# Performance work log

Hardware: AMD Instinct MI355X
Metric: run time of the kernel (lower is better)

Reference implementation:

```python
import jax, jax.numpy as jnp
import numpy as np

NODE_DIM = 512
PROMPT_DIM = 512
N_NODES = 100000
N_GRAPHS = 1024


def setup_inputs() -> dict:
    key = jax.random.key(0)
    k1, k2, k3, k4, k5, k6, k7 = jax.random.split(key, 7)
    node_feats = jax.random.normal(k1, (N_NODES, NODE_DIM), dtype=jnp.float32)
    graph_prompt = jax.random.normal(k2, (N_GRAPHS, PROMPT_DIM), dtype=jnp.float32)
    batch_idx = jnp.sort(jax.random.randint(k3, (N_NODES,), 0, N_GRAPHS))
    # Linear init ~ U(-1/sqrt(fan_in), 1/sqrt(fan_in)) like torch defaults
    fan1 = NODE_DIM + PROMPT_DIM
    b1 = 1.0 / np.sqrt(fan1)
    W1 = jax.random.uniform(k4, (fan1, NODE_DIM), minval=-b1, maxval=b1, dtype=jnp.float32)
    bias1 = jax.random.uniform(k5, (NODE_DIM,), minval=-b1, maxval=b1, dtype=jnp.float32)
    b2 = 1.0 / np.sqrt(NODE_DIM)
    W2 = jax.random.uniform(k6, (NODE_DIM, NODE_DIM), minval=-b2, maxval=b2, dtype=jnp.float32)
    bias2 = jax.random.uniform(k7, (NODE_DIM,), minval=-b2, maxval=b2, dtype=jnp.float32)
    return {"node_feats": node_feats, "graph_prompt": graph_prompt, "batch_idx": batch_idx,
            "W1": W1, "bias1": bias1, "W2": W2, "bias2": bias2}


def reference(node_feats, graph_prompt, batch_idx, W1, bias1, W2, bias2):
    # gather per-node prompt: [N, prompt_dim]
    prompt_expanded = graph_prompt[batch_idx]
    combined = jnp.concatenate([node_feats, prompt_expanded], axis=-1)  # [N, node_dim+prompt_dim]
    h = jax.nn.relu(combined @ W1 + bias1)  # [N, node_dim]
    return h @ W2 + bias2  # [N, node_dim]
```

## Files before the change

### kernel.cpp

```cpp
#include <hip/hip_runtime.h>


#define N_NODES 100000
#define NWG 3128

typedef __bf16 bf16x8 __attribute__((ext_vector_type(8)));
typedef float  f32x4  __attribute__((ext_vector_type(4)));
typedef unsigned short ushort_t;

__device__ __forceinline__ ushort_t f2bf(float f) {
  __bf16 b = (__bf16)f;
  return __builtin_bit_cast(unsigned short, b);
}

__device__ __forceinline__ bf16x8 cvt8(const float* p) {
  float4 x = *(const float4*)p;
  float4 y = *(const float4*)(p + 4);
  bf16x8 v;
  v[0] = (__bf16)x.x; v[1] = (__bf16)x.y; v[2] = (__bf16)x.z; v[3] = (__bf16)x.w;
  v[4] = (__bf16)y.x; v[5] = (__bf16)y.y; v[6] = (__bf16)y.z; v[7] = (__bf16)y.w;
  return v;
}

__device__ __forceinline__ bf16x8 cvt8v(float4 x, float4 y) {
  bf16x8 v;
  v[0] = (__bf16)x.x; v[1] = (__bf16)x.y; v[2] = (__bf16)x.z; v[3] = (__bf16)x.w;
  v[4] = (__bf16)y.x; v[5] = (__bf16)y.y; v[6] = (__bf16)y.z; v[7] = (__bf16)y.w;
  return v;
}

__device__ __forceinline__ void gload_lds16(const void* g, void* l) {
  __builtin_amdgcn_global_load_lds(
      (const __attribute__((address_space(1))) void*)g,
      (__attribute__((address_space(3))) void*)l, 16, 0, 0);
}

__global__ void prep_kernel(const float* __restrict__ W1, const float* __restrict__ W2,
                            ushort_t* __restrict__ W1T, ushort_t* __restrict__ W2T) {
  int i = blockIdx.x * 256 + threadIdx.x;
  if (i < 524288) {
    int n = i >> 10, k = i & 1023;
    W1T[i] = f2bf(W1[k * 512 + n]);
  } else if (i < 786432) {
    int j = i - 524288;
    int n = j >> 9, k = j & 511;
    W2T[j] = f2bf(W2[k * 512 + n]);
  }
}

__global__ __launch_bounds__(256, 4) void p2_kernel(
    const float* __restrict__ gp, const ushort_t* __restrict__ W1T,
    const float* __restrict__ bias1, float* __restrict__ P2) {
  const int tid = threadIdx.x, lane = tid & 63, wid = tid >> 6;
  const int lc = lane & 15, lr = lane >> 4;
  const int m0 = (blockIdx.x >> 1) * 32;
  const int col0 = (blockIdx.x & 1) * 256 + wid * 64;

  f32x4 acc[2][4];
#pragma unroll
  for (int i = 0; i < 2; ++i)
#pragma unroll
    for (int j = 0; j < 4; ++j) acc[i][j] = {0.f, 0.f, 0.f, 0.f};

  const float* a0 = gp + (size_t)(m0 + lc) * 512;
  const ushort_t* bb = W1T + (size_t)(col0 + lc) * 1024 + 512;

#pragma unroll 2
  for (int kt = 0; kt < 8; ++kt) {
    bf16x8 bfr[2][4];
#pragma unroll
    for (int kk = 0; kk < 2; ++kk)
#pragma unroll
      for (int j = 0; j < 4; ++j)
        bfr[kk][j] = *(const bf16x8*)(bb + (size_t)j * 16 * 1024 + kt * 64 + kk * 32 + lr * 8);
    bf16x8 af[2][2];
#pragma unroll
    for (int i = 0; i < 2; ++i)
#pragma unroll
      for (int kk = 0; kk < 2; ++kk)
        af[i][kk] = cvt8(a0 + (size_t)i * 16 * 512 + kt * 64 + kk * 32 + lr * 8);
#pragma unroll
    for (int kk = 0; kk < 2; ++kk)
#pragma unroll
      for (int i = 0; i < 2; ++i)
#pragma unroll
        for (int j = 0; j < 4; ++j)
          acc[i][j] = __builtin_amdgcn_mfma_f32_16x16x32_bf16(af[i][kk], bfr[kk][j], acc[i][j], 0, 0, 0);
  }

#pragma unroll
  for (int i = 0; i < 2; ++i)
#pragma unroll
    for (int r = 0; r < 4; ++r) {
      int row = m0 + i * 16 + lr * 4 + r;
#pragma unroll
      for (int j = 0; j < 4; ++j) {
        int col = col0 + j * 16 + lc;
        P2[(size_t)row * 512 + col] = acc[i][j][r] + bias1[col];
      }
    }
}

__global__ __launch_bounds__(256, 4) void g1_kernel(
    const float* __restrict__ nf, const int* __restrict__ bidx,
    const ushort_t* __restrict__ W1T, const float* __restrict__ P2,
    ushort_t* __restrict__ h) {
  __shared__ ushort_t sA[128 * 64];
  __shared__ ushort_t sB[128 * 64];

  const int tid = threadIdx.x, lane = tid & 63, wid = tid >> 6;
  const int tile = (blockIdx.x & 7) * 391 + (blockIdx.x >> 3);
  const int m0 = (tile >> 2) * 128, n0 = (tile & 3) * 128;

  const float* pAg[4]; int ldsA[4];
#pragma unroll
  for (int s = 0; s < 4; ++s) {
    int q = s * 256 + tid;
    int row = q >> 3;
    int cw = (q & 7) ^ (row & 7);
    int rowg = m0 + row; if (rowg > N_NODES - 1) rowg = N_NODES - 1;
    pAg[s] = nf + (size_t)rowg * 512 + cw * 8;
    ldsA[s] = q * 8;
  }
  const ushort_t* pB[4]; int ldsB[4];
#pragma unroll
  for (int s = 0; s < 4; ++s) {
    int q = wid * 256 + s * 64 + lane;
    int row = q >> 3;
    int cw = (q & 7) ^ (row & 7);
    pB[s] = W1T + (size_t)(n0 + row) * 1024 + cw * 8;
    ldsB[s] = (wid * 256 + s * 64) * 8;
  }

  f32x4 acc[4][4];
#pragma unroll
  for (int i = 0; i < 4; ++i)
#pragma unroll
    for (int j = 0; j < 4; ++j) acc[i][j] = {0.f, 0.f, 0.f, 0.f};

  const int wm = (wid >> 1) * 64, wn = (wid & 1) * 64;
  const int lr = lane >> 4, lc = lane & 15;

  for (int kt = 0; kt < 8; ++kt) {
    float4 ax[4], ay[4];
#pragma unroll
    for (int s = 0; s < 4; ++s) {
      ax[s] = *(const float4*)(pAg[s]);
      ay[s] = *(const float4*)(pAg[s] + 4);
      pAg[s] += 64;
    }
#pragma unroll
    for (int s = 0; s < 4; ++s) { gload_lds16(pB[s], &sB[ldsB[s]]); pB[s] += 64; }
#pragma unroll
    for (int s = 0; s < 4; ++s)
      *(bf16x8*)&sA[ldsA[s]] = cvt8v(ax[s], ay[s]);
    __syncthreads();

#pragma unroll
    for (int kk = 0; kk < 2; ++kk) {
      bf16x8 af[4], bfr[4];
#pragma unroll
      for (int i = 0; i < 4; ++i) {
        int row = wm + i * 16 + lc;
        int cp = (kk * 4 + lr) ^ (row & 7);
        af[i] = *(const bf16x8*)&sA[row * 64 + cp * 8];
      }
#pragma unroll
      for (int j = 0; j < 4; ++j) {
        int col = wn + j * 16 + lc;
        int cp = (kk * 4 + lr) ^ (col & 7);
        bfr[j] = *(const bf16x8*)&sB[col * 64 + cp * 8];
      }
#pragma unroll
      for (int i = 0; i < 4; ++i)
#pragma unroll
        for (int j = 0; j < 4; ++j)
          acc[i][j] = __builtin_amdgcn_mfma_f32_16x16x32_bf16(af[i], bfr[j], acc[i][j], 0, 0, 0);
    }
    __syncthreads();
  }

#pragma unroll
  for (int i = 0; i < 4; ++i) {
#pragma unroll
    for (int r = 0; r < 4; ++r) {
      int row = m0 + wm + i * 16 + lr * 4 + r;
      if (row < N_NODES) {
        int g = bidx[row];
        const float* p2r = P2 + (size_t)g * 512 + n0 + wn;
#pragma unroll
        for (int j = 0; j < 4; ++j) {
          float v = fmaxf(acc[i][j][r] + p2r[j * 16 + lc], 0.f);
          h[(size_t)row * 512 + n0 + wn + j * 16 + lc] = f2bf(v);
        }
      }
    }
  }
}

__global__ __launch_bounds__(256, 4) void g2_kernel(
    const ushort_t* __restrict__ h, const ushort_t* __restrict__ W2T,
    const float* __restrict__ bias2, float* __restrict__ out) {
  __shared__ ushort_t sA[128 * 64];
  __shared__ ushort_t sB[128 * 64];

  const int tid = threadIdx.x, lane = tid & 63, wid = tid >> 6;
  const int tile = (blockIdx.x & 7) * 391 + (blockIdx.x >> 3);
  const int m0 = (tile >> 2) * 128, n0 = (tile & 3) * 128;

  const ushort_t* pA[4]; const ushort_t* pB[4]; int ldsW[4];
#pragma unroll
  for (int s = 0; s < 4; ++s) {
    int q = wid * 256 + s * 64 + lane;
    int row = q >> 3;
    int cw = (q & 7) ^ (row & 7);
    int rowg = m0 + row; if (rowg > N_NODES - 1) rowg = N_NODES - 1;
    pA[s] = h + (size_t)rowg * 512 + cw * 8;
    pB[s] = W2T + (size_t)(n0 + row) * 512 + cw * 8;
    ldsW[s] = (wid * 256 + s * 64) * 8;
  }

  f32x4 acc[4][4];
#pragma unroll
  for (int i = 0; i < 4; ++i)
#pragma unroll
    for (int j = 0; j < 4; ++j) acc[i][j] = {0.f, 0.f, 0.f, 0.f};

  const int wm = (wid >> 1) * 64, wn = (wid & 1) * 64;
  const int lr = lane >> 4, lc = lane & 15;

  for (int kt = 0; kt < 8; ++kt) {
#pragma unroll
    for (int s = 0; s < 4; ++s) {
      gload_lds16(pA[s], &sA[ldsW[s]]); pA[s] += 64;
      gload_lds16(pB[s], &sB[ldsW[s]]); pB[s] += 64;
    }
    __syncthreads();
#pragma unroll
    for (int kk = 0; kk < 2; ++kk) {
      bf16x8 af[4], bfr[4];
#pragma unroll
      for (int i = 0; i < 4; ++i) {
        int row = wm + i * 16 + lc;
        int cp = (kk * 4 + lr) ^ (row & 7);
        af[i] = *(const bf16x8*)&sA[row * 64 + cp * 8];
      }
#pragma unroll
      for (int j = 0; j < 4; ++j) {
        int col = wn + j * 16 + lc;
        int cp = (kk * 4 + lr) ^ (col & 7);
        bfr[j] = *(const bf16x8*)&sB[col * 64 + cp * 8];
      }
#pragma unroll
      for (int i = 0; i < 4; ++i)
#pragma unroll
        for (int j = 0; j < 4; ++j)
          acc[i][j] = __builtin_amdgcn_mfma_f32_16x16x32_bf16(af[i], bfr[j], acc[i][j], 0, 0, 0);
    }
    __syncthreads();
  }

#pragma unroll
  for (int j = 0; j < 4; ++j) {
    int col = n0 + wn + j * 16 + lc;
    float bv = bias2[col];
#pragma unroll
    for (int i = 0; i < 4; ++i)
#pragma unroll
      for (int r = 0; r < 4; ++r) {
        int row = m0 + wm + i * 16 + lr * 4 + r;
        if (row < N_NODES) out[(size_t)row * 512 + col] = acc[i][j][r] + bv;
      }
  }
}

extern "C" void kernel_launch(void* const* d_in, const int* in_sizes, int n_in,
                              void* d_out, int out_size, void* d_ws, size_t ws_size,
                              hipStream_t stream) {
  const float* nf   = (const float*)d_in[0];
  const float* gp   = (const float*)d_in[1];
  const int*   bidx = (const int*)d_in[2];
  const float* W1   = (const float*)d_in[3];
  const float* b1   = (const float*)d_in[4];
  const float* W2   = (const float*)d_in[5];
  const float* b2   = (const float*)d_in[6];
  float* out = (float*)d_out;

  char* ws = (char*)d_ws;
  ushort_t* W1T = (ushort_t*)ws;
  ushort_t* W2T = (ushort_t*)(ws + 1048576);
  float*    P2  = (float*)   (ws + 1572864);
  ushort_t* hbf = (ushort_t*)(ws + 3670016);

  prep_kernel<<<3072, 256, 0, stream>>>(W1, W2, W1T, W2T);
  p2_kernel<<<64, 256, 0, stream>>>(gp, W1T, b1, P2);
  g1_kernel<<<NWG, 256, 0, stream>>>(nf, bidx, W1T, P2, hbf);
  g2_kernel<<<NWG, 256, 0, stream>>>(hbf, W2T, b2, out);
}
```

Baseline: 276.5 us.

## Widen GEMM tiles to 128x256 with 512-thread blocks and XCD tile mapping

Both node GEMMs now use 128x256 output tiles computed by 8 waves per block instead of 128x128 tiles with 4 waves, which halves the number of workgroups. Each A tile (node features or h) is loaded once per 256 columns rather than per 128, cutting redundant A reads and fp32 to bf16 conversions in g1. A new XCD-aware block-to-tile mapping keeps neighbouring M tiles on the same XCD. The cost is larger LDS per block and possibly lower occupancy, plus a coarser grid that may tail worse across CUs.

```diff
diff --git a/kernel.cpp b/kernel.cpp
--- a/kernel.cpp
+++ b/kernel.cpp
@@ -2,7 +2,7 @@
 
 
 #define N_NODES 100000
-#define NWG 3128
+#define NWG 1564
 
 typedef __bf16 bf16x8 __attribute__((ext_vector_type(8)));
 typedef float  f32x4  __attribute__((ext_vector_type(4)));
@@ -33,6 +33,11 @@
   __builtin_amdgcn_global_load_lds(
       (const __attribute__((address_space(1))) void*)g,
       (__attribute__((address_space(3))) void*)l, 16, 0, 0);
+}
+
+__device__ __forceinline__ int xcd_map(int b) {
+  int xcd = b & 7, pos = b >> 3;
+  return (xcd < 4 ? xcd * 196 : 784 + (xcd - 4) * 195) + pos;
 }
 
 __global__ void prep_kernel(const float* __restrict__ W1, const float* __restrict__ W2,
@@ -101,21 +106,21 @@
     }
 }
 
-__global__ __launch_bounds__(256, 4) void g1_kernel(
+__global__ __launch_bounds__(512, 4) void g1_kernel(
     const float* __restrict__ nf, const int* __restrict__ bidx,
     const ushort_t* __restrict__ W1T, const float* __restrict__ P2,
     ushort_t* __restrict__ h) {
   __shared__ ushort_t sA[128 * 64];
-  __shared__ ushort_t sB[128 * 64];
+  __shared__ ushort_t sB[256 * 64];
 
   const int tid = threadIdx.x, lane = tid & 63, wid = tid >> 6;
-  const int tile = (blockIdx.x & 7) * 391 + (blockIdx.x >> 3);
-  const int m0 = (tile >> 2) * 128, n0 = (tile & 3) * 128;
-
-  const float* pAg[4]; int ldsA[4];
-#pragma unroll
-  for (int s = 0; s < 4; ++s) {
-    int q = s * 256 + tid;
+  const int wg = xcd_map(blockIdx.x);
+  const int m0 = (wg >> 1) * 128, n0 = (wg & 1) * 256;
+
+  const float* pAg[2]; int ldsA[2];
+#pragma unroll
+  for (int s = 0; s < 2; ++s) {
+    int q = s * 512 + tid;
     int row = q >> 3;
     int cw = (q & 7) ^ (row & 7);
     int rowg = m0 + row; if (rowg > N_NODES - 1) rowg = N_NODES - 1;
@@ -138,13 +143,14 @@
 #pragma unroll
     for (int j = 0; j < 4; ++j) acc[i][j] = {0.f, 0.f, 0.f, 0.f};
 
-  const int wm = (wid >> 1) * 64, wn = (wid & 1) * 64;
+  const int wm = (wid >> 2) * 64;
+  const int wn = (wid & 3) * 64;
   const int lr = lane >> 4, lc = lane & 15;
 
   for (int kt = 0; kt < 8; ++kt) {
-    float4 ax[4], ay[4];
-#pragma unroll
-    for (int s = 0; s < 4; ++s) {
+    float4 ax[2], ay[2];
+#pragma unroll
+    for (int s = 0; s < 2; ++s) {
       ax[s] = *(const float4*)(pAg[s]);
       ay[s] = *(const float4*)(pAg[s] + 4);
       pAg[s] += 64;
@@ -152,7 +158,7 @@
 #pragma unroll
     for (int s = 0; s < 4; ++s) { gload_lds16(pB[s], &sB[ldsB[s]]); pB[s] += 64; }
 #pragma unroll
-    for (int s = 0; s < 4; ++s)
+    for (int s = 0; s < 2; ++s)
       *(bf16x8*)&sA[ldsA[s]] = cvt8v(ax[s], ay[s]);
     __syncthreads();
 
@@ -198,26 +204,34 @@
   }
 }
 
-__global__ __launch_bounds__(256, 4) void g2_kernel(
+__global__ __launch_bounds__(512, 4) void g2_kernel(
     const ushort_t* __restrict__ h, const ushort_t* __restrict__ W2T,
     const float* __restrict__ bias2, float* __restrict__ out) {
   __shared__ ushort_t sA[128 * 64];
-  __shared__ ushort_t sB[128 * 64];
+  __shared__ ushort_t sB[256 * 64];
 
   const int tid = threadIdx.x, lane = tid & 63, wid = tid >> 6;
-  const int tile = (blockIdx.x & 7) * 391 + (blockIdx.x >> 3);
-  const int m0 = (tile >> 2) * 128, n0 = (tile & 3) * 128;
-
-  const ushort_t* pA[4]; const ushort_t* pB[4]; int ldsW[4];
+  const int wg = xcd_map(blockIdx.x);
+  const int m0 = (wg >> 1) * 128, n0 = (wg & 1) * 256;
+
+  const ushort_t* pA[2]; int ldsA[2];
+#pragma unroll
+  for (int s = 0; s < 2; ++s) {
+    int q = s * 512 + tid;
+    int row = q >> 3;
+    int cw = (q & 7) ^ (row & 7);
+    int rowg = m0 + row; if (rowg > N_NODES - 1) rowg = N_NODES - 1;
+    pA[s] = h + (size_t)rowg * 512 + cw * 8;
+    ldsA[s] = (s * 512 + wid * 64) * 8;
+  }
+  const ushort_t* pB[4]; int ldsB[4];
 #pragma unroll
   for (int s = 0; s < 4; ++s) {
     int q = wid * 256 + s * 64 + lane;
     int row = q >> 3;
     int cw = (q & 7) ^ (row & 7);
-    int rowg = m0 + row; if (rowg > N_NODES - 1) rowg = N_NODES - 1;
-    pA[s] = h + (size_t)rowg * 512 + cw * 8;
     pB[s] = W2T + (size_t)(n0 + row) * 512 + cw * 8;
-    ldsW[s] = (wid * 256 + s * 64) * 8;
+    ldsB[s] = (wid * 256 + s * 64) * 8;
   }
 
   f32x4 acc[4][4];
@@ -226,16 +240,17 @@
 #pragma unroll
     for (int j = 0; j < 4; ++j) acc[i][j] = {0.f, 0.f, 0.f, 0.f};
 
-  const int wm = (wid >> 1) * 64, wn = (wid & 1) * 64;
+  const int wm = (wid >> 2) * 64;
+  const int wn = (wid & 3) * 64;
   const int lr = lane >> 4, lc = lane & 15;
 
   for (int kt = 0; kt < 8; ++kt) {
 #pragma unroll
-    for (int s = 0; s < 4; ++s) {
-      gload_lds16(pA[s], &sA[ldsW[s]]); pA[s] += 64;
-      gload_lds16(pB[s], &sB[ldsW[s]]); pB[s] += 64;
-    }
+    for (int s = 0; s < 2; ++s) { gload_lds16(pA[s], &sA[ldsA[s]]); pA[s] += 64; }
+#pragma unroll
+    for (int s = 0; s < 4; ++s) { gload_lds16(pB[s], &sB[ldsB[s]]); pB[s] += 64; }
     __syncthreads();
+
 #pragma unroll
     for (int kk = 0; kk < 2; ++kk) {
       bf16x8 af[4], bfr[4];
@@ -294,6 +309,6 @@
 
   prep_kernel<<<3072, 256, 0, stream>>>(W1, W2, W1T, W2T);
   p2_kernel<<<64, 256, 0, stream>>>(gp, W1T, b1, P2);
-  g1_kernel<<<NWG, 256, 0, stream>>>(nf, bidx, W1T, P2, hbf);
-  g2_kernel<<<NWG, 256, 0, stream>>>(hbf, W2T, b2, out);
-}
+  g1_kernel<<<NWG, 512, 0, stream>>>(nf, bidx, W1T, P2, hbf);
+  g2_kernel<<<NWG, 512, 0, stream>>>(hbf, W2T, b2, out);
+}
```

Result: no change. 281.1 us (+1.7%).
